# Performance work log

Hardware: AMD Instinct MI355X
Metric: run time of the kernel (lower is better)

## Reference

```python
import jax, jax.numpy as jnp
import numpy as np

B, N, D = 8, 2048, 1024

def setup_inputs() -> dict:
    key = jax.random.key(0)
    ks = jax.random.split(key, 7)
    s = 1.0 / np.sqrt(D)
    return {
        "x": jax.random.normal(ks[0], (B, N, D), dtype=jnp.float32),
        "Wq": jax.random.uniform(ks[1], (D, D), jnp.float32, -s, s),
        "bq": jax.random.uniform(ks[2], (D,), jnp.float32, -s, s),
        "Wk": jax.random.uniform(ks[3], (D, D), jnp.float32, -s, s),
        "bk": jax.random.uniform(ks[4], (D,), jnp.float32, -s, s),
        "Wv": jax.random.uniform(ks[5], (D, D), jnp.float32, -s, s),
        "bv": jax.random.uniform(ks[6], (D,), jnp.float32, -s, s),
    }

def reference(x, Wq, bq, Wk, bk, Wv, bv):
    # torch nn.Linear: y = x @ W.T + b
    q = jnp.einsum('bnd,ed->bne', x, Wq) + bq
    k = jnp.einsum('bnd,ed->bne', x, Wk) + bk
    v = jnp.einsum('bnd,ed->bne', x, Wv) + bv
    # NOTE: original applies NO 1/sqrt(d) scaling
    scores = jnp.einsum('bnd,bmd->bnm', q, k)  # [B, N, N]
    probs = jax.nn.softmax(scores, axis=-1)
    return jnp.einsum('bnm,bmd->bnd', probs, v)
```

## Files before the change

kernel.cpp:

```cpp
#include <hip/hip_runtime.h>


typedef _Float16 f16;
typedef _Float16 f16x4 __attribute__((ext_vector_type(4)));
typedef _Float16 f16x8 __attribute__((ext_vector_type(8)));
typedef float f32x4 __attribute__((ext_vector_type(4)));

#define Nn_ 2048
#define Dd 1024

typedef const __attribute__((address_space(1))) void gvoid;
typedef __attribute__((address_space(3))) void lvoid;

__device__ __forceinline__ void glds16(const void* g, void* l) {
    __builtin_amdgcn_global_load_lds((gvoid*)g, (lvoid*)l, 16, 0, 0);
}
#define BARRIER()  asm volatile("s_barrier" ::: "memory")
#define LGKM0()    asm volatile("s_waitcnt lgkmcnt(0)" ::: "memory")
#define VM6()      asm volatile("s_waitcnt vmcnt(6)" ::: "memory")
#define VM0()      asm volatile("s_waitcnt vmcnt(0)" ::: "memory")
#define PRIO1()    __builtin_amdgcn_s_setprio(1)
#define PRIO0()    __builtin_amdgcn_s_setprio(0)
#define MFMA(a, b, c) __builtin_amdgcn_mfma_f32_16x16x32_f16((a), (b), (c), 0, 0, 0)

__global__ void cvt_kernel(const float4* __restrict__ in, f16x4* __restrict__ out, int n4) {
    int i = blockIdx.x * 256 + threadIdx.x;
    if (i >= n4) return;
    float4 f = in[i];
    f16x4 h;
    h.x = (_Float16)f.x; h.y = (_Float16)f.y; h.z = (_Float16)f.z; h.w = (_Float16)f.w;
    out[i] = h;
}

__global__ void concat_bias(const float* __restrict__ bq, const float* __restrict__ bk,
                            const float* __restrict__ bv, float* __restrict__ o) {
    int i = blockIdx.x * 256 + threadIdx.x;
    if (i >= 3072) return;
    o[i] = (i < 1024) ? bq[i] : (i < 2048 ? bk[i - 1024] : bv[i - 2048]);
}

__global__ __launch_bounds__(512) void gemm_bt(
    const f16* __restrict__ A, const f16* __restrict__ Bm,
    const float* __restrict__ bias, void* __restrict__ Cout,
    f16* __restrict__ qh, f16* __restrict__ kh, f16* __restrict__ vT,
    int K, int lda, int ldb, int ldc, int mode,
    long aStride, long bStride, long cStride)
{
    __shared__ f16 sm[65536];
    const int tid = threadIdx.x;
    const int lane = tid & 63, wid = tid >> 6;
    const int quad = lane >> 4, l16 = lane & 15;
    const int wm = wid & 1;
    const int wn = wid >> 1;
    const long m0 = (long)blockIdx.x * 256, n0 = (long)blockIdx.y * 256;
    A += (long)blockIdx.z * aStride;
    Bm += (long)blockIdx.z * bStride;

    const int lr = tid >> 3;
    const int sc8 = ((tid & 7) ^ (lr & 7)) * 8;
    const f16* pa = A + (m0 + lr) * (long)lda + sc8;
    const f16* pb = Bm + (n0 + lr) * (long)ldb + sc8;
    const long a64 = 64L * lda, b64 = 64L * ldb;

    const int aRow = (wm * 128 + l16) * 64;
    const int bRow = (wn * 64 + l16) * 64;
    const int co0 = (quad ^ (l16 & 7)) * 8;
    const int co1 = ((quad + 4) ^ (l16 & 7)) * 8;

    f32x4 acc[8][4];
#pragma unroll
    for (int i = 0; i < 8; i++)
#pragma unroll
        for (int j = 0; j < 4; j++) acc[i][j] = 0.0f;

    const int nk = K >> 6;

#pragma unroll
    for (int q = 0; q < 4; ++q) glds16(pa + q * a64, sm + tid * 8 + q * 4096);
#pragma unroll
    for (int q = 0; q < 4; ++q) glds16(pb + q * b64, sm + 16384 + tid * 8 + q * 4096);
    if (nk > 1) {
        glds16(pa + 0 * a64 + 64, sm + 32768 + tid * 8);
        glds16(pa + 2 * a64 + 64, sm + 32768 + tid * 8 + 2 * 4096);
#pragma unroll
        for (int q = 0; q < 4; ++q)
            glds16(pb + q * b64 + 64, sm + 32768 + 16384 + tid * 8 + q * 4096);
        VM6(); BARRIER();
    } else {
        VM0(); BARRIER();
    }

    f16x8 af[2][4], bf0[2][2], bf1[2][2];
    for (int t = 0; t < nk; ++t) {
        const int bo = (t & 1) << 15;
        const int bn = bo ^ 32768;
        const f16* As = sm + bo;
        const f16* Bs = As + 16384;
        const long kt1 = (long)(t + 1) * 64, kt2 = (long)(t + 2) * 64;

#pragma unroll
        for (int i = 0; i < 4; ++i) {
            af[0][i] = *(const f16x8*)(As + aRow + i * 1024 + co0);
            af[1][i] = *(const f16x8*)(As + aRow + i * 1024 + co1);
        }
#pragma unroll
        for (int j = 0; j < 2; ++j) {
            bf0[0][j] = *(const f16x8*)(Bs + bRow + j * 1024 + co0);
            bf0[1][j] = *(const f16x8*)(Bs + bRow + j * 1024 + co1);
        }
        if (t + 1 < nk) {
            glds16(pa + 1 * a64 + kt1, sm + bn + tid * 8 + 1 * 4096);
            glds16(pa + 3 * a64 + kt1, sm + bn + tid * 8 + 3 * 4096);
        }
        BARRIER(); LGKM0(); PRIO1();
#pragma unroll
        for (int i = 0; i < 4; ++i)
#pragma unroll
            for (int j = 0; j < 2; ++j) {
                acc[i][j] = MFMA(af[0][i], bf0[0][j], acc[i][j]);
                acc[i][j] = MFMA(af[1][i], bf0[1][j], acc[i][j]);
            }
        PRIO0(); BARRIER();

#pragma unroll
        for (int j = 0; j < 2; ++j) {
            bf1[0][j] = *(const f16x8*)(Bs + bRow + 2048 + j * 1024 + co0);
            bf1[1][j] = *(const f16x8*)(Bs + bRow + 2048 + j * 1024 + co1);
        }
        if (t + 2 < nk) {
            glds16(pa + 0 * a64 + kt2, sm + bo + tid * 8);
            glds16(pa + 2 * a64 + kt2, sm + bo + tid * 8 + 2 * 4096);
        }
        BARRIER(); LGKM0(); PRIO1();
#pragma unroll
        for (int i = 0; i < 4; ++i)
#pragma unroll
            for (int j = 0; j < 2; ++j) {
                acc[i][2 + j] = MFMA(af[0][i], bf1[0][j], acc[i][2 + j]);
                acc[i][2 + j] = MFMA(af[1][i], bf1[1][j], acc[i][2 + j]);
            }
        PRIO0(); BARRIER();

#pragma unroll
        for (int i = 0; i < 4; ++i) {
            af[0][i] = *(const f16x8*)(As + aRow + 4096 + i * 1024 + co0);
            af[1][i] = *(const f16x8*)(As + aRow + 4096 + i * 1024 + co1);
        }
        if (t + 2 < nk) {
            glds16(pb + 0 * b64 + kt2, sm + bo + 16384 + tid * 8);
            glds16(pb + 1 * b64 + kt2, sm + bo + 16384 + tid * 8 + 4096);
        }
        BARRIER(); LGKM0(); PRIO1();
#pragma unroll
        for (int i = 0; i < 4; ++i)
#pragma unroll
            for (int j = 0; j < 2; ++j) {
                acc[4 + i][j] = MFMA(af[0][i], bf0[0][j], acc[4 + i][j]);
                acc[4 + i][j] = MFMA(af[1][i], bf0[1][j], acc[4 + i][j]);
            }
        PRIO0(); BARRIER();

        if (t + 2 < nk) {
            glds16(pb + 2 * b64 + kt2, sm + bo + 16384 + tid * 8 + 2 * 4096);
            glds16(pb + 3 * b64 + kt2, sm + bo + 16384 + tid * 8 + 3 * 4096);
        }
        BARRIER(); PRIO1();
#pragma unroll
        for (int i = 0; i < 4; ++i)
#pragma unroll
            for (int j = 0; j < 2; ++j) {
                acc[4 + i][2 + j] = MFMA(af[0][i], bf1[0][j], acc[4 + i][2 + j]);
                acc[4 + i][2 + j] = MFMA(af[1][i], bf1[1][j], acc[4 + i][2 + j]);
            }
        PRIO0();
        if (t + 2 < nk) { VM6(); } else { VM0(); }
        BARRIER();
    }

    if (mode == 2) {
        float* O = (float*)Cout + (long)blockIdx.z * cStride;
#pragma unroll
        for (int ct = 0; ct < 4; ct++) {
            long n = n0 + wn * 64 + ct * 16 + l16;
#pragma unroll
            for (int rt = 0; rt < 8; rt++) {
                long mb = m0 + wm * 128 + rt * 16 + quad * 4;
#pragma unroll
                for (int r = 0; r < 4; r++)
                    O[(mb + r) * ldc + n] = acc[rt][ct][r];
            }
        }
    } else {
        if (blockIdx.y < 8) {
            f16* O = (blockIdx.y < 4) ? qh : kh;
#pragma unroll
            for (int ct = 0; ct < 4; ct++) {
                long n = n0 + wn * 64 + ct * 16 + l16;
                float bs = bias[n];
                long n1 = n & 1023;
#pragma unroll
                for (int rt = 0; rt < 8; rt++) {
                    long mb = m0 + wm * 128 + rt * 16 + quad * 4;
#pragma unroll
                    for (int r = 0; r < 4; r++)
                        O[(mb + r) * 1024 + n1] = (f16)(acc[rt][ct][r] + bs);
                }
            }
        } else {
            const long nb = n0 - 2048;
            const long vbase = (m0 >> 11) * (long)(Dd * Nn_) + (m0 & 2047);
#pragma unroll
            for (int g = 0; g < 4; ++g) {
                __syncthreads();
                if (wn == g) {
#pragma unroll
                    for (int ct = 0; ct < 4; ++ct) {
                        int cl = ct * 16 + l16;
                        float bs = bias[n0 + g * 64 + cl];
#pragma unroll
                        for (int rt = 0; rt < 8; rt++) {
                            int row = wm * 128 + rt * 16 + quad * 4;
#pragma unroll
                            for (int r = 0; r < 4; r++)
                                sm[cl * 264 + row + r] = (f16)(acc[rt][ct][r] + bs);
                        }
                    }
                }
                __syncthreads();
                const int rowi = tid >> 3, c = (tid & 7) * 32;
                f16* dst = vT + vbase + (nb + g * 64 + rowi) * (long)Nn_ + c;
                const f16* src = sm + rowi * 264 + c;
                *(f16x8*)(dst) = *(const f16x8*)(src);
                *(f16x8*)(dst + 8) = *(const f16x8*)(src + 8);
                *(f16x8*)(dst + 16) = *(const f16x8*)(src + 16);
                *(f16x8*)(dst + 24) = *(const f16x8*)(src + 24);
            }
        }
    }
}

__global__ __launch_bounds__(256) void softmax_rows(float* __restrict__ S) {
    const int row = blockIdx.x * 4 + (threadIdx.x >> 6);
    const int lane = threadIdx.x & 63;
    float* Sr = S + (long)row * 2048;
    const float4* R4 = (const float4*)Sr;
    float4 t[8];
#pragma unroll
    for (int i = 0; i < 8; i++) t[i] = R4[lane + 64 * i];
    float mx = -1e30f;
#pragma unroll
    for (int i = 0; i < 8; i++)
        mx = fmaxf(mx, fmaxf(fmaxf(t[i].x, t[i].y), fmaxf(t[i].z, t[i].w)));
#pragma unroll
    for (int off = 1; off < 64; off <<= 1) mx = fmaxf(mx, __shfl_xor(mx, off, 64));
    float se = 0.0f;
#pragma unroll
    for (int i = 0; i < 8; i++) {
        t[i].x = __expf(t[i].x - mx); t[i].y = __expf(t[i].y - mx);
        t[i].z = __expf(t[i].z - mx); t[i].w = __expf(t[i].w - mx);
        se += t[i].x + t[i].y + t[i].z + t[i].w;
    }
#pragma unroll
    for (int off = 1; off < 64; off <<= 1) se += __shfl_xor(se, off, 64);
    const float li = 1.0f / se;
    f16x4* P4 = (f16x4*)Sr;
#pragma unroll
    for (int i = 0; i < 8; i++) {
        f16x4 h;
        h.x = (_Float16)(t[i].x * li); h.y = (_Float16)(t[i].y * li);
        h.z = (_Float16)(t[i].z * li); h.w = (_Float16)(t[i].w * li);
        P4[lane + 64 * i] = h;
    }
}

extern "C" void kernel_launch(void* const* d_in, const int* in_sizes, int n_in,
                              void* d_out, int out_size, void* d_ws, size_t ws_size,
                              hipStream_t stream) {
    const float* x  = (const float*)d_in[0];
    const float* Wq = (const float*)d_in[1];
    const float* bq = (const float*)d_in[2];
    const float* Wk = (const float*)d_in[3];
    const float* bk = (const float*)d_in[4];
    const float* Wv = (const float*)d_in[5];
    const float* bv = (const float*)d_in[6];

    f16* wsh = (f16*)d_ws;
    dim3 blk(512);
    const bool full = ws_size >= 234881024ULL;

    if (full) {
        f16* qh  = wsh;
        f16* kh  = wsh + 16777216;
        f16* vT  = wsh + 33554432;
        float* S = (float*)(wsh + 50331648);
        f16* xh  = wsh + 50331648;
        f16* Wh  = wsh + 67108864;
        float* bqkv = (float*)(wsh + 70254592);

        cvt_kernel<<<16384, 256, 0, stream>>>((const float4*)x, (f16x4*)xh, 4194304);
        cvt_kernel<<<1024, 256, 0, stream>>>((const float4*)Wq, (f16x4*)Wh, 262144);
        cvt_kernel<<<1024, 256, 0, stream>>>((const float4*)Wk, (f16x4*)(Wh + 1048576), 262144);
        cvt_kernel<<<1024, 256, 0, stream>>>((const float4*)Wv, (f16x4*)(Wh + 2097152), 262144);
        concat_bias<<<12, 256, 0, stream>>>(bq, bk, bv, bqkv);

        gemm_bt<<<dim3(64, 12, 1), blk, 0, stream>>>(
            xh, Wh, bqkv, nullptr, qh, kh, vT,
            1024, 1024, 1024, 0, 3, 0, 0, 0);
        gemm_bt<<<dim3(8, 8, 8), blk, 0, stream>>>(
            qh, kh, nullptr, S, nullptr, nullptr, nullptr,
            1024, 1024, 1024, 2048, 2,
            (long)Nn_ * Dd, (long)Nn_ * Dd, (long)Nn_ * Nn_);
        softmax_rows<<<4096, 256, 0, stream>>>(S);
        gemm_bt<<<dim3(8, 4, 8), blk, 0, stream>>>(
            (const f16*)S, vT, nullptr, d_out, nullptr, nullptr, nullptr,
            2048, 4096, 2048, 1024, 2,
            (long)Nn_ * 4096, (long)Dd * Nn_, (long)Nn_ * Dd);
    } else {
        f16* xh  = wsh;
        f16* Wh  = wsh + 16777216;
        float* bqkv = (float*)(wsh + 19922944);
        f16* qh  = wsh + 19929088;
        f16* kh  = qh + 16777216;
        f16* vT  = kh + 16777216;
        float* S = (float*)(vT + 16777216);

        cvt_kernel<<<16384, 256, 0, stream>>>((const float4*)x, (f16x4*)xh, 4194304);
        cvt_kernel<<<1024, 256, 0, stream>>>((const float4*)Wq, (f16x4*)Wh, 262144);
        cvt_kernel<<<1024, 256, 0, stream>>>((const float4*)Wk, (f16x4*)(Wh + 1048576), 262144);
        cvt_kernel<<<1024, 256, 0, stream>>>((const float4*)Wv, (f16x4*)(Wh + 2097152), 262144);
        concat_bias<<<12, 256, 0, stream>>>(bq, bk, bv, bqkv);

        gemm_bt<<<dim3(64, 12, 1), blk, 0, stream>>>(
            xh, Wh, bqkv, nullptr, qh, kh, vT,
            1024, 1024, 1024, 0, 3, 0, 0, 0);

        for (int h = 0; h < 2; ++h) {
            const long b0 = 4L * h;
            gemm_bt<<<dim3(8, 8, 4), blk, 0, stream>>>(
                qh + b0 * Nn_ * Dd, kh + b0 * Nn_ * Dd, nullptr, S,
                nullptr, nullptr, nullptr,
                1024, 1024, 1024, 2048, 2,
                (long)Nn_ * Dd, (long)Nn_ * Dd, (long)Nn_ * Nn_);
            softmax_rows<<<2048, 256, 0, stream>>>(S);
            gemm_bt<<<dim3(8, 4, 4), blk, 0, stream>>>(
                (const f16*)S, vT + b0 * Dd * Nn_, nullptr,
                (float*)d_out + b0 * Nn_ * Dd, nullptr, nullptr, nullptr,
                2048, 4096, 2048, 1024, 2,
                (long)Nn_ * 4096, (long)Dd * Nn_, (long)Nn_ * Dd);
        }
    }
}
```

Measured before the change: 434.2 us.

## Software-pipeline LDS fragment reads so each MFMA block overlaps the next loads

Restructures the GEMM main loop so LDS fragment reads for the next quarter-tile are issued before the current MFMA block runs. The A-fragment registers are split into af0 and af1, and the next tile's first fragments are prefetched at the end of each iteration. This removes the read-then-wait-then-compute serialization and cuts one barrier per phase. In exchange it uses more VGPRs, which could lower occupancy, and reorders the global-to-LDS stage issue, which needs correct barrier and waitcnt placement.

```diff
diff --git a/kernel.cpp b/kernel.cpp
--- a/kernel.cpp
+++ b/kernel.cpp
@@ -80,101 +80,127 @@
 #pragma unroll
     for (int q = 0; q < 4; ++q) glds16(pb + q * b64, sm + 16384 + tid * 8 + q * 4096);
     if (nk > 1) {
-        glds16(pa + 0 * a64 + 64, sm + 32768 + tid * 8);
-        glds16(pa + 2 * a64 + 64, sm + 32768 + tid * 8 + 2 * 4096);
 #pragma unroll
         for (int q = 0; q < 4; ++q)
-            glds16(pb + q * b64 + 64, sm + 32768 + 16384 + tid * 8 + q * 4096);
-        VM6(); BARRIER();
+            glds16(pa + q * a64 + 64, sm + 32768 + tid * 8 + q * 4096);
+#pragma unroll
+        for (int q = 0; q < 4; ++q)
+            glds16(pb + q * b64 + 64, sm + 49152 + tid * 8 + q * 4096);
+        VM6();
     } else {
-        VM0(); BARRIER();
-    }
-
-    f16x8 af[2][4], bf0[2][2], bf1[2][2];
-    for (int t = 0; t < nk; ++t) {
-        const int bo = (t & 1) << 15;
-        const int bn = bo ^ 32768;
-        const f16* As = sm + bo;
-        const f16* Bs = As + 16384;
-        const long kt1 = (long)(t + 1) * 64, kt2 = (long)(t + 2) * 64;
-
+        VM0();
+    }
+    BARRIER();
+
+    f16x8 af0[2][4], af1[2][4], bf0[2][2], bf1[2][2];
+    {
+        const f16* As = sm;
+        const f16* Bs = sm + 16384;
 #pragma unroll
         for (int i = 0; i < 4; ++i) {
-            af[0][i] = *(const f16x8*)(As + aRow + i * 1024 + co0);
-            af[1][i] = *(const f16x8*)(As + aRow + i * 1024 + co1);
+            af0[0][i] = *(const f16x8*)(As + aRow + i * 1024 + co0);
+            af0[1][i] = *(const f16x8*)(As + aRow + i * 1024 + co1);
         }
 #pragma unroll
         for (int j = 0; j < 2; ++j) {
             bf0[0][j] = *(const f16x8*)(Bs + bRow + j * 1024 + co0);
             bf0[1][j] = *(const f16x8*)(Bs + bRow + j * 1024 + co1);
         }
-        if (t + 1 < nk) {
-            glds16(pa + 1 * a64 + kt1, sm + bn + tid * 8 + 1 * 4096);
-            glds16(pa + 3 * a64 + kt1, sm + bn + tid * 8 + 3 * 4096);
-        }
-        BARRIER(); LGKM0(); PRIO1();
-#pragma unroll
-        for (int i = 0; i < 4; ++i)
-#pragma unroll
-            for (int j = 0; j < 2; ++j) {
-                acc[i][j] = MFMA(af[0][i], bf0[0][j], acc[i][j]);
-                acc[i][j] = MFMA(af[1][i], bf0[1][j], acc[i][j]);
-            }
-        PRIO0(); BARRIER();
-
+    }
+    LGKM0();
+
+    int bo = 0;
+    for (int t = 0; t < nk; ++t) {
+        const f16* As = sm + bo;
+        const f16* Bs = As + 16384;
+        const f16* An = sm + (bo ^ 32768);
+        const f16* Bn = An + 16384;
+        const long kt2 = (long)(t + 2) * 64;
+        const bool st = (t + 2) < nk;
+
+        BARRIER();
 #pragma unroll
         for (int j = 0; j < 2; ++j) {
             bf1[0][j] = *(const f16x8*)(Bs + bRow + 2048 + j * 1024 + co0);
             bf1[1][j] = *(const f16x8*)(Bs + bRow + 2048 + j * 1024 + co1);
         }
-        if (t + 2 < nk) {
+        if (st) {
             glds16(pa + 0 * a64 + kt2, sm + bo + tid * 8);
             glds16(pa + 2 * a64 + kt2, sm + bo + tid * 8 + 2 * 4096);
         }
-        BARRIER(); LGKM0(); PRIO1();
+        PRIO1();
 #pragma unroll
         for (int i = 0; i < 4; ++i)
 #pragma unroll
             for (int j = 0; j < 2; ++j) {
-                acc[i][2 + j] = MFMA(af[0][i], bf1[0][j], acc[i][2 + j]);
-                acc[i][2 + j] = MFMA(af[1][i], bf1[1][j], acc[i][2 + j]);
-            }
-        PRIO0(); BARRIER();
-
+                acc[i][j] = MFMA(af0[0][i], bf0[0][j], acc[i][j]);
+                acc[i][j] = MFMA(af0[1][i], bf0[1][j], acc[i][j]);
+            }
+        PRIO0(); LGKM0();
+
+        BARRIER();
 #pragma unroll
         for (int i = 0; i < 4; ++i) {
-            af[0][i] = *(const f16x8*)(As + aRow + 4096 + i * 1024 + co0);
-            af[1][i] = *(const f16x8*)(As + aRow + 4096 + i * 1024 + co1);
-        }
-        if (t + 2 < nk) {
+            af1[0][i] = *(const f16x8*)(As + aRow + 4096 + i * 1024 + co0);
+            af1[1][i] = *(const f16x8*)(As + aRow + 4096 + i * 1024 + co1);
+        }
+        if (st) {
             glds16(pb + 0 * b64 + kt2, sm + bo + 16384 + tid * 8);
             glds16(pb + 1 * b64 + kt2, sm + bo + 16384 + tid * 8 + 4096);
         }
-        BARRIER(); LGKM0(); PRIO1();
+        PRIO1();
 #pragma unroll
         for (int i = 0; i < 4; ++i)
 #pragma unroll
             for (int j = 0; j < 2; ++j) {
-                acc[4 + i][j] = MFMA(af[0][i], bf0[0][j], acc[4 + i][j]);
-                acc[4 + i][j] = MFMA(af[1][i], bf0[1][j], acc[4 + i][j]);
-            }
-        PRIO0(); BARRIER();
-
-        if (t + 2 < nk) {
+                acc[i][2 + j] = MFMA(af0[0][i], bf1[0][j], acc[i][2 + j]);
+                acc[i][2 + j] = MFMA(af0[1][i], bf1[1][j], acc[i][2 + j]);
+            }
+        PRIO0(); LGKM0();
+
+        BARRIER();
+        if (st) {
             glds16(pb + 2 * b64 + kt2, sm + bo + 16384 + tid * 8 + 2 * 4096);
             glds16(pb + 3 * b64 + kt2, sm + bo + 16384 + tid * 8 + 3 * 4096);
         }
-        BARRIER(); PRIO1();
+        PRIO1();
 #pragma unroll
         for (int i = 0; i < 4; ++i)
 #pragma unroll
             for (int j = 0; j < 2; ++j) {
-                acc[4 + i][2 + j] = MFMA(af[0][i], bf1[0][j], acc[4 + i][2 + j]);
-                acc[4 + i][2 + j] = MFMA(af[1][i], bf1[1][j], acc[4 + i][2 + j]);
+                acc[4 + i][j] = MFMA(af1[0][i], bf0[0][j], acc[4 + i][j]);
+                acc[4 + i][j] = MFMA(af1[1][i], bf0[1][j], acc[4 + i][j]);
             }
         PRIO0();
-        if (t + 2 < nk) { VM6(); } else { VM0(); }
+        if (st) { VM6(); } else { VM0(); }
+
         BARRIER();
+        if (t + 1 < nk) {
+#pragma unroll
+            for (int i = 0; i < 4; ++i) {
+                af0[0][i] = *(const f16x8*)(An + aRow + i * 1024 + co0);
+                af0[1][i] = *(const f16x8*)(An + aRow + i * 1024 + co1);
+            }
+#pragma unroll
+            for (int j = 0; j < 2; ++j) {
+                bf0[0][j] = *(const f16x8*)(Bn + bRow + j * 1024 + co0);
+                bf0[1][j] = *(const f16x8*)(Bn + bRow + j * 1024 + co1);
+            }
+        }
+        if (st) {
+            glds16(pa + 1 * a64 + kt2, sm + bo + tid * 8 + 4096);
+            glds16(pa + 3 * a64 + kt2, sm + bo + tid * 8 + 3 * 4096);
+        }
+        PRIO1();
+#pragma unroll
+        for (int i = 0; i < 4; ++i)
+#pragma unroll
+            for (int j = 0; j < 2; ++j) {
+                acc[4 + i][2 + j] = MFMA(af1[0][i], bf1[0][j], acc[4 + i][2 + j]);
+                acc[4 + i][2 + j] = MFMA(af1[1][i], bf1[1][j], acc[4 + i][2 + j]);
+            }
+        PRIO0(); LGKM0();
+        bo ^= 32768;
     }
 
     if (mode == 2) {
```

After: 435.3 us. About the same (+0.2%).
